# Kernel optimization log

Hardware: AMD Instinct MI355X
Metric: run time of the kernel (lower is better)

The kernel has to match this reference:

```python
import jax, jax.numpy as jnp
import numpy as np


def setup_inputs() -> dict:
    key = jax.random.key(0)
    k1, k2 = jax.random.split(key)
    N, C, H, W = 64, 1024, 28, 28
    x = jax.random.normal(k1, (N, C, H, W), dtype=jnp.float32)
    fc_weights = jax.random.normal(k2, (C,), dtype=jnp.float32)
    mu = jnp.float32(0.7)
    return {"x": x, "fc_weights": fc_weights, "mu": mu}


def reference(x, fc_weights, mu):
    # cams = relu(x * w_c), shape [N, C, H, W]
    cams = jax.nn.relu(x * fc_weights.reshape(1, -1, 1, 1))
    # per-(sample, channel) spatial max -> threshold
    cam_max = jnp.max(cams, axis=(2, 3), keepdims=True)        # [N, C, 1, 1]
    thr = cam_max * mu
    # drop (zero out) high-activation regions, keep the rest
    dropped = jnp.where(cams > thr, jnp.zeros_like(cams), cams)
    # accumulate over channels -> [N, 1, H, W]
    mean_drop_cam = jnp.sum(dropped, axis=1, keepdims=True)
    return x * mean_drop_cam
```

## Files before the change

kernel.cpp:

```cpp
#include <hip/hip_runtime.h>

#define HWD 784
#define Q4  196
#define CD  1024
#define ND  64

#define CHPB 32
#define NCHUNK (CD / CHPB)

typedef float f32x4 __attribute__((ext_vector_type(4)));

__device__ __forceinline__ float4 cam4(float4 v, float wc) {
    float4 r;
    r.x = fmaxf(v.x * wc, 0.f);
    r.y = fmaxf(v.y * wc, 0.f);
    r.z = fmaxf(v.z * wc, 0.f);
    r.w = fmaxf(v.w * wc, 0.f);
    return r;
}
__device__ __forceinline__ float max4(float4 v) {
    return fmaxf(fmaxf(v.x, v.y), fmaxf(v.z, v.w));
}
__device__ __forceinline__ void accdrop(float4& a, float4 c, float thr) {
    a.x += (c.x > thr) ? 0.f : c.x;
    a.y += (c.y > thr) ? 0.f : c.y;
    a.z += (c.z > thr) ? 0.f : c.z;
    a.w += (c.w > thr) ? 0.f : c.w;
}

__global__ void __launch_bounds__(256) pass1_kernel(const float* __restrict__ x,
                                                    const float* __restrict__ w,
                                                    const float* __restrict__ mu_p,
                                                    float* __restrict__ Spart) {
    __shared__ float4 drp[4][197];

    const int t = threadIdx.x;
    const int wave = t >> 6;
    const int lane = t & 63;
    const int n = blockIdx.y;
    const int cbase = blockIdx.x * CHPB + wave * 8;
    const float mu = mu_p[0];

    const float4* rows = reinterpret_cast<const float4*>(x + ((size_t)n * CD + cbase) * HWD);

    float4 acc0 = {0.f,0.f,0.f,0.f}, acc1 = {0.f,0.f,0.f,0.f};
    float4 acc2 = {0.f,0.f,0.f,0.f}, acc3 = {0.f,0.f,0.f,0.f};

    #pragma unroll
    for (int ph = 0; ph < 2; ++ph) {
        const float4* r0 = rows + (ph * 4) * Q4;
        const float4* r1 = r0 + Q4;
        const float4* r2 = r1 + Q4;
        const float4* r3 = r2 + Q4;
        float4 a0 = r0[lane], a1 = r0[lane + 64], a2 = r0[lane + 128];
        float4 b0 = r1[lane], b1 = r1[lane + 64], b2 = r1[lane + 128];
        float4 c0 = r2[lane], c1 = r2[lane + 64], c2 = r2[lane + 128];
        float4 d0 = r3[lane], d1 = r3[lane + 64], d2 = r3[lane + 128];
        float4 a3 = {0.f,0.f,0.f,0.f}, b3 = {0.f,0.f,0.f,0.f};
        float4 c3 = {0.f,0.f,0.f,0.f}, d3 = {0.f,0.f,0.f,0.f};
        if (lane < 4) {
            a3 = r0[192 + lane]; b3 = r1[192 + lane];
            c3 = r2[192 + lane]; d3 = r3[192 + lane];
        }

        const float w0 = w[cbase + ph * 4 + 0];
        const float w1 = w[cbase + ph * 4 + 1];
        const float w2 = w[cbase + ph * 4 + 2];
        const float w3 = w[cbase + ph * 4 + 3];

        a0 = cam4(a0, w0); a1 = cam4(a1, w0); a2 = cam4(a2, w0); a3 = cam4(a3, w0);
        b0 = cam4(b0, w1); b1 = cam4(b1, w1); b2 = cam4(b2, w1); b3 = cam4(b3, w1);
        c0 = cam4(c0, w2); c1 = cam4(c1, w2); c2 = cam4(c2, w2); c3 = cam4(c3, w2);
        d0 = cam4(d0, w3); d1 = cam4(d1, w3); d2 = cam4(d2, w3); d3 = cam4(d3, w3);

        float m0 = fmaxf(fmaxf(max4(a0), max4(a1)), fmaxf(max4(a2), max4(a3)));
        float m1 = fmaxf(fmaxf(max4(b0), max4(b1)), fmaxf(max4(b2), max4(b3)));
        float m2 = fmaxf(fmaxf(max4(c0), max4(c1)), fmaxf(max4(c2), max4(c3)));
        float m3 = fmaxf(fmaxf(max4(d0), max4(d1)), fmaxf(max4(d2), max4(d3)));

        #pragma unroll
        for (int off = 32; off > 0; off >>= 1) {
            m0 = fmaxf(m0, __shfl_xor(m0, off, 64));
            m1 = fmaxf(m1, __shfl_xor(m1, off, 64));
            m2 = fmaxf(m2, __shfl_xor(m2, off, 64));
            m3 = fmaxf(m3, __shfl_xor(m3, off, 64));
        }
        const float t0 = m0 * mu, t1 = m1 * mu, t2 = m2 * mu, t3 = m3 * mu;

        accdrop(acc0, a0, t0); accdrop(acc1, a1, t0); accdrop(acc2, a2, t0); accdrop(acc3, a3, t0);
        accdrop(acc0, b0, t1); accdrop(acc1, b1, t1); accdrop(acc2, b2, t1); accdrop(acc3, b3, t1);
        accdrop(acc0, c0, t2); accdrop(acc1, c1, t2); accdrop(acc2, c2, t2); accdrop(acc3, c3, t2);
        accdrop(acc0, d0, t3); accdrop(acc1, d1, t3); accdrop(acc2, d2, t3); accdrop(acc3, d3, t3);
    }

    drp[wave][lane]       = acc0;
    drp[wave][64 + lane]  = acc1;
    drp[wave][128 + lane] = acc2;
    if (lane < 4) drp[wave][192 + lane] = acc3;
    __syncthreads();

    const float* f = reinterpret_cast<const float*>(&drp[0][0]);
    float* sp = Spart + ((size_t)blockIdx.x * ND + n) * HWD;
    for (int p = t; p < HWD; p += 256)
        sp[p] = f[p] + f[788 + p] + f[2 * 788 + p] + f[3 * 788 + p];
}

__global__ void __launch_bounds__(256) reduce_kernel(const float* __restrict__ Spart,
                                                     float* __restrict__ S) {
    const int j = blockIdx.x * 256 + threadIdx.x;
    float s = 0.f;
    #pragma unroll
    for (int ch = 0; ch < NCHUNK; ++ch)
        s += Spart[(size_t)ch * ND * HWD + j];
    S[j] = s;
}

__global__ void __launch_bounds__(256) mult_kernel(const float* __restrict__ x,
                                                   const float* __restrict__ S,
                                                   float* __restrict__ out) {
    const float4* x4 = reinterpret_cast<const float4*>(x);
    const float4* S4 = reinterpret_cast<const float4*>(S);

    int i4 = blockIdx.x * 256 + threadIdx.x;
    #pragma unroll 4
    for (int it = 0; it < 16; ++it, i4 += 3136 * 256) {
        const int r = i4 / Q4;
        const int p4 = i4 - r * Q4;
        const int n = r >> 10;
        float4 xv = x4[i4];
        float4 sv = S4[n * Q4 + p4];
        float4 o;
        o.x = xv.x * sv.x;
        o.y = xv.y * sv.y;
        o.z = xv.z * sv.z;
        o.w = xv.w * sv.w;
        __builtin_nontemporal_store(*reinterpret_cast<const f32x4*>(&o),
                                    reinterpret_cast<f32x4*>(out) + i4);
    }
}

extern "C" void kernel_launch(void* const* d_in, const int* in_sizes, int n_in,
                              void* d_out, int out_size, void* d_ws, size_t ws_size,
                              hipStream_t stream) {
    const float* x  = (const float*)d_in[0];
    const float* w  = (const float*)d_in[1];
    const float* mu = (const float*)d_in[2];
    float* out = (float*)d_out;

    float* Spart = (float*)d_ws;
    float* S     = Spart + (size_t)NCHUNK * ND * HWD;

    dim3 g1(NCHUNK, ND);
    pass1_kernel<<<g1, 256, 0, stream>>>(x, w, mu, Spart);

    reduce_kernel<<<ND * HWD / 256, 256, 0, stream>>>(Spart, S);

    mult_kernel<<<3136, 256, 0, stream>>>(x, S, out);
}
```

Measured before the change: 101.1 us.

## Fuse partial-sum reduction into multiply kernel and remap pass1 blocks per XCD

Removes the separate reduce kernel: each multiply block sums the 32 channel-chunk partials for its 16 spatial positions into LDS, then scales 1024 channels of x. The multiply is reorganised so each block covers a fixed sample and position group, striding across channels. Pass1 blocks are launched on a 1D grid with a swizzle that gives each of 8 groups a contiguous range of work, presumably to keep locality per XCD. This saves one launch and the S round trip. In exchange, the multiply kernel does 64-byte scattered accesses at a stride of HWD, which coalesces worse, and it recomputes the reduction redundantly per block.

```diff
diff --git a/kernel.cpp b/kernel.cpp
--- a/kernel.cpp
+++ b/kernel.cpp
@@ -7,6 +7,7 @@
 
 #define CHPB 32
 #define NCHUNK (CD / CHPB)
+#define NBLK (NCHUNK * ND)
 
 typedef float f32x4 __attribute__((ext_vector_type(4)));
 
@@ -34,11 +35,14 @@
                                                     float* __restrict__ Spart) {
     __shared__ float4 drp[4][197];
 
+    const int bid = blockIdx.x;
+    const int work = (bid & 7) * (NBLK / 8) + (bid >> 3);
+    const int n = work >> 5;
+    const int chunk = work & 31;
     const int t = threadIdx.x;
     const int wave = t >> 6;
     const int lane = t & 63;
-    const int n = blockIdx.y;
-    const int cbase = blockIdx.x * CHPB + wave * 8;
+    const int cbase = chunk * CHPB + wave * 8;
     const float mu = mu_p[0];
 
     const float4* rows = reinterpret_cast<const float4*>(x + ((size_t)n * CD + cbase) * HWD);
@@ -100,42 +104,45 @@
     __syncthreads();
 
     const float* f = reinterpret_cast<const float*>(&drp[0][0]);
-    float* sp = Spart + ((size_t)blockIdx.x * ND + n) * HWD;
+    float* sp = Spart + ((size_t)chunk * ND + n) * HWD;
     for (int p = t; p < HWD; p += 256)
         sp[p] = f[p] + f[788 + p] + f[2 * 788 + p] + f[3 * 788 + p];
 }
 
-__global__ void __launch_bounds__(256) reduce_kernel(const float* __restrict__ Spart,
-                                                     float* __restrict__ S) {
-    const int j = blockIdx.x * 256 + threadIdx.x;
-    float s = 0.f;
-    #pragma unroll
-    for (int ch = 0; ch < NCHUNK; ++ch)
-        s += Spart[(size_t)ch * ND * HWD + j];
-    S[j] = s;
-}
+__global__ void __launch_bounds__(256) mult_kernel(const float* __restrict__ x,
+                                                   const float* __restrict__ Spart,
+                                                   float* __restrict__ out) {
+    __shared__ float S_lds[16];
 
-__global__ void __launch_bounds__(256) mult_kernel(const float* __restrict__ x,
-                                                   const float* __restrict__ S,
-                                                   float* __restrict__ out) {
-    const float4* x4 = reinterpret_cast<const float4*>(x);
-    const float4* S4 = reinterpret_cast<const float4*>(S);
+    const int t = threadIdx.x;
+    const int n = blockIdx.y;
+    const int pos0 = blockIdx.x * 16;
 
-    int i4 = blockIdx.x * 256 + threadIdx.x;
+    if (t < 16) {
+        float s = 0.f;
+        #pragma unroll
+        for (int ch = 0; ch < NCHUNK; ++ch)
+            s += Spart[((size_t)ch * ND + n) * HWD + pos0 + t];
+        S_lds[t] = s;
+    }
+    __syncthreads();
+
+    const int q = t & 3;
+    const int g = t >> 2;
+    const float4 sv = *reinterpret_cast<const float4*>(S_lds + q * 4);
+    const size_t base = (size_t)n * CD * HWD + pos0 + q * 4;
+
     #pragma unroll 4
-    for (int it = 0; it < 16; ++it, i4 += 3136 * 256) {
-        const int r = i4 / Q4;
-        const int p4 = i4 - r * Q4;
-        const int n = r >> 10;
-        float4 xv = x4[i4];
-        float4 sv = S4[n * Q4 + p4];
+    for (int k = 0; k < 16; ++k) {
+        const size_t idx = base + (size_t)(g + (k << 6)) * HWD;
+        float4 xv = *reinterpret_cast<const float4*>(x + idx);
         float4 o;
         o.x = xv.x * sv.x;
         o.y = xv.y * sv.y;
         o.z = xv.z * sv.z;
         o.w = xv.w * sv.w;
         __builtin_nontemporal_store(*reinterpret_cast<const f32x4*>(&o),
-                                    reinterpret_cast<f32x4*>(out) + i4);
+                                    reinterpret_cast<f32x4*>(out + idx));
     }
 }
 
@@ -148,12 +155,9 @@
     float* out = (float*)d_out;
 
     float* Spart = (float*)d_ws;
-    float* S     = Spart + (size_t)NCHUNK * ND * HWD;
 
-    dim3 g1(NCHUNK, ND);
-    pass1_kernel<<<g1, 256, 0, stream>>>(x, w, mu, Spart);
+    pass1_kernel<<<NBLK, 256, 0, stream>>>(x, w, mu, Spart);
 
-    reduce_kernel<<<ND * HWD / 256, 256, 0, stream>>>(Spart, S);
-
-    mult_kernel<<<3136, 256, 0, stream>>>(x, S, out);
+    dim3 gm(HWD / 16, ND);
+    mult_kernel<<<gm, 256, 0, stream>>>(x, Spart, out);
 }
```

New measurement: 128.5 us. 27.1% more time.
